# Kernel tuning notes

Hardware: AMD Instinct MI355X
Metric: run time of the kernel (lower is better)

The kernel has to match this reference:

```python
import jax, jax.numpy as jnp
import numpy as np

H = 8          # n_channels
NEIGHBORS = 5


def setup_inputs() -> dict:
    key = jax.random.key(0)
    k1, k2 = jax.random.split(key)
    B, N, C = 8, 1024, 256
    x = jax.random.normal(k1, (B, N, C), dtype=jnp.float32)
    # torch Linear weight: [out_features, in_features] = [2*H*C, C]
    W_qk = jax.random.normal(k2, (2 * H * C, C), dtype=jnp.float32) * (C ** -0.5)
    return {"x": x, "W_qk": W_qk}


def _forward(x, W_qk):
    B, N, C = x.shape
    scale = C ** -0.5
    qk = (x @ W_qk.T).reshape(B, N, 2, H, C).transpose(2, 0, 3, 1, 4)
    q, k = qk[0], qk[1]                              # [B,H,N,C]
    attn = jax.nn.softmax(jnp.einsum('bhnc,bhmc->bhnm', q, k) * scale, axis=-1)

    # clip(): top-k on detached channel-summed attention
    sum_edge = jnp.sum(jax.lax.stop_gradient(attn), axis=1)   # [B,N,N]
    _, index = jax.lax.top_k(sum_edge, NEIGHBORS)             # [B,N,NEIGHBORS]
    # Faithful to source: every mask row gets 1 at the union of ALL rows'
    # top-k indices (inner loop iterates over all rows of `inds`), plus eye(N).
    flat_idx = index.reshape(B, N * NEIGHBORS)                # [B, N*nb]
    col_mask = jnp.zeros((B, N), dtype=attn.dtype).at[
        jnp.arange(B)[:, None], flat_idx].set(1.0)            # [B,N]
    mask = jnp.maximum(jnp.eye(N, dtype=attn.dtype)[None], col_mask[:, None, :])  # [B,N,N]

    new_edge = mask[:, None] * attn                           # [B,H,N,N]

    # norm_edge(): row norm, then col norm, then row @ col^T
    norm_row = new_edge / (jnp.sum(new_edge, axis=-1, keepdims=True) + 1e-16)
    norm_col = norm_row / (jnp.sum(norm_row, axis=-2, keepdims=True) + 1e-16)
    return jnp.einsum('bhnm,bhkm->bhnk', norm_row, norm_col)  # [B,H,N,N]


def reference(x, W_qk):
    return _forward(x, W_qk)
```

## Files before the change

### kernel.cpp

```cpp
#include <hip/hip_runtime.h>
#include <hip/hip_bf16.h>
#include <cstdint>
#include <cstddef>

#define BB 8
#define HH 8
#define NN 1024
#define CC 256
#define OUTCH 4096

typedef __attribute__((ext_vector_type(8))) __bf16 bf16x8;
typedef __attribute__((ext_vector_type(4))) __bf16 bf16x4;
typedef __attribute__((ext_vector_type(4))) float f32x4;

__device__ inline void async16(const void* g, void* l)
{
  __builtin_amdgcn_global_load_lds(
      reinterpret_cast<const __attribute__((address_space(1))) unsigned int*>(
          reinterpret_cast<uintptr_t>(g)),
      reinterpret_cast<__attribute__((address_space(3))) unsigned int*>(
          reinterpret_cast<uintptr_t>(l)),
      16, 0, 0);
}

__device__ inline float waveMax(float v) {
#pragma unroll
  for (int o = 32; o > 0; o >>= 1) v = fmaxf(v, __shfl_xor(v, o, 64));
  return v;
}
__device__ inline float waveSum(float v) {
#pragma unroll
  for (int o = 32; o > 0; o >>= 1) v += __shfl_xor(v, o, 64);
  return v;
}

__global__ __launch_bounds__(256) void split_kernel(const float* __restrict__ in,
                                                    __bf16* __restrict__ hi,
                                                    __bf16* __restrict__ lo, int n4)
{
  const int i = blockIdx.x * 256 + threadIdx.x;
  if (i >= n4) return;
  const float4 v = ((const float4*)in)[i];
  bf16x4 h, l;
  h.x = (__bf16)v.x; l.x = (__bf16)(v.x - (float)h.x);
  h.y = (__bf16)v.y; l.y = (__bf16)(v.y - (float)h.y);
  h.z = (__bf16)v.z; l.z = (__bf16)(v.z - (float)h.z);
  h.w = (__bf16)v.w; l.w = (__bf16)(v.w - (float)h.w);
  ((bf16x4*)hi)[i] = h;
  ((bf16x4*)lo)[i] = l;
}

__global__ __launch_bounds__(256) void xw_mfma_kernel(
    const __bf16* __restrict__ Ah, const __bf16* __restrict__ Al,
    const __bf16* __restrict__ Bh, const __bf16* __restrict__ Bl,
    __bf16* __restrict__ Chi, __bf16* __restrict__ Clo)
{
  __shared__ __bf16 AsH[128 * 32], AsL[128 * 32], BsH[128 * 32], BsL[128 * 32];

  const int tid = threadIdx.x, lane = tid & 63, wid = tid >> 6;
  const int wr = wid >> 1, wc = wid & 1;
  const int bM = blockIdx.y * 128, bN = blockIdx.x * 128;

  const int srow = wid * 16 + (lane >> 2);
  const int scol = (lane & 3) * 8;
  const __bf16* gAh = Ah + (size_t)(bM + srow) * CC + scol;
  const __bf16* gAl = Al + (size_t)(bM + srow) * CC + scol;
  const __bf16* gBh = Bh + (size_t)(bN + srow) * CC + scol;
  const __bf16* gBl = Bl + (size_t)(bN + srow) * CC + scol;
  char* lAh = (char*)AsH + wid * 16 * 64;
  char* lAl = (char*)AsL + wid * 16 * 64;
  char* lBh = (char*)BsH + wid * 16 * 64;
  char* lBl = (char*)BsL + wid * 16 * 64;

  f32x4 acc[4][4];
  const f32x4 z = {0.f, 0.f, 0.f, 0.f};
#pragma unroll
  for (int m = 0; m < 4; ++m)
#pragma unroll
    for (int n = 0; n < 4; ++n) acc[m][n] = z;

  for (int k0 = 0; k0 < CC; k0 += 32) {
    async16(gAh + k0, lAh); async16(gAh + k0 + 64 * CC, lAh + 64 * 64);
    async16(gAl + k0, lAl); async16(gAl + k0 + 64 * CC, lAl + 64 * 64);
    async16(gBh + k0, lBh); async16(gBh + k0 + 64 * CC, lBh + 64 * 64);
    async16(gBl + k0, lBl); async16(gBl + k0 + 64 * CC, lBl + 64 * 64);
    __syncthreads();

    bf16x8 ah[4], al[4], bh_[4], bl_[4];
    const int fb = (lane & 15) * 64 + (lane >> 4) * 16;
#pragma unroll
    for (int m = 0; m < 4; ++m) {
      ah[m] = *(const bf16x8*)((const char*)AsH + (wr * 64 + m * 16) * 64 + fb);
      al[m] = *(const bf16x8*)((const char*)AsL + (wr * 64 + m * 16) * 64 + fb);
    }
#pragma unroll
    for (int n = 0; n < 4; ++n) {
      bh_[n] = *(const bf16x8*)((const char*)BsH + (wc * 64 + n * 16) * 64 + fb);
      bl_[n] = *(const bf16x8*)((const char*)BsL + (wc * 64 + n * 16) * 64 + fb);
    }
#pragma unroll
    for (int m = 0; m < 4; ++m)
#pragma unroll
      for (int n = 0; n < 4; ++n) {
        acc[m][n] = __builtin_amdgcn_mfma_f32_16x16x32_bf16(al[m], bh_[n], acc[m][n], 0, 0, 0);
        acc[m][n] = __builtin_amdgcn_mfma_f32_16x16x32_bf16(ah[m], bl_[n], acc[m][n], 0, 0, 0);
        acc[m][n] = __builtin_amdgcn_mfma_f32_16x16x32_bf16(ah[m], bh_[n], acc[m][n], 0, 0, 0);
      }
    __syncthreads();
  }

  const int fr = lane & 15;
  const int fq = lane >> 4;
#pragma unroll
  for (int m = 0; m < 4; ++m) {
    const int row0 = bM + wr * 64 + m * 16 + fq * 4;
#pragma unroll
    for (int n = 0; n < 4; ++n) {
      const int col = bN + wc * 64 + n * 16 + fr;
#pragma unroll
      for (int r = 0; r < 4; ++r) {
        const float v = acc[m][n][r];
        const __bf16 h = (__bf16)v;
        const __bf16 l = (__bf16)(v - (float)h);
        Chi[(size_t)(row0 + r) * OUTCH + col] = h;
        Clo[(size_t)(row0 + r) * OUTCH + col] = l;
      }
    }
  }
}

__global__ __launch_bounds__(256) void qkt_mfma_kernel(
    const __bf16* __restrict__ Qh, const __bf16* __restrict__ Ql,
    float* __restrict__ outall)
{
  const int f = blockIdx.x;
  const int xcd = f & 7;
  const int g = f >> 3;
  const int bh = xcd + 8 * (g >> 6);
  const int tile = g & 63;
  const int b = bh >> 3, h = bh & 7;
  const size_t qoff = (size_t)b * NN * OUTCH + (size_t)h * CC;
  const size_t koff = qoff + 2048;
  float* C = outall + ((size_t)bh << 20);

  __shared__ __bf16 AsH[128 * 32], AsL[128 * 32], BsH[128 * 32], BsL[128 * 32];

  const int tid = threadIdx.x, lane = tid & 63, wid = tid >> 6;
  const int wr = wid >> 1, wc = wid & 1;
  const int bM = (tile >> 3) * 128, bN = (tile & 7) * 128;

  const int srow = wid * 16 + (lane >> 2);
  const int scol = (lane & 3) * 8;
  const __bf16* gAh = Qh + qoff + (size_t)(bM + srow) * OUTCH + scol;
  const __bf16* gAl = Ql + qoff + (size_t)(bM + srow) * OUTCH + scol;
  const __bf16* gBh = Qh + koff + (size_t)(bN + srow) * OUTCH + scol;
  const __bf16* gBl = Ql + koff + (size_t)(bN + srow) * OUTCH + scol;
  char* lAh = (char*)AsH + wid * 16 * 64;
  char* lAl = (char*)AsL + wid * 16 * 64;
  char* lBh = (char*)BsH + wid * 16 * 64;
  char* lBl = (char*)BsL + wid * 16 * 64;

  f32x4 acc[4][4];
  const f32x4 z = {0.f, 0.f, 0.f, 0.f};
#pragma unroll
  for (int m = 0; m < 4; ++m)
#pragma unroll
    for (int n = 0; n < 4; ++n) acc[m][n] = z;

  for (int k0 = 0; k0 < CC; k0 += 32) {
    async16(gAh + k0, lAh); async16(gAh + k0 + (size_t)64 * OUTCH, lAh + 64 * 64);
    async16(gAl + k0, lAl); async16(gAl + k0 + (size_t)64 * OUTCH, lAl + 64 * 64);
    async16(gBh + k0, lBh); async16(gBh + k0 + (size_t)64 * OUTCH, lBh + 64 * 64);
    async16(gBl + k0, lBl); async16(gBl + k0 + (size_t)64 * OUTCH, lBl + 64 * 64);
    __syncthreads();

    bf16x8 ah[4], al[4], bh_[4], bl_[4];
    const int fb = (lane & 15) * 64 + (lane >> 4) * 16;
#pragma unroll
    for (int m = 0; m < 4; ++m) {
      ah[m] = *(const bf16x8*)((const char*)AsH + (wr * 64 + m * 16) * 64 + fb);
      al[m] = *(const bf16x8*)((const char*)AsL + (wr * 64 + m * 16) * 64 + fb);
    }
#pragma unroll
    for (int n = 0; n < 4; ++n) {
      bh_[n] = *(const bf16x8*)((const char*)BsH + (wc * 64 + n * 16) * 64 + fb);
      bl_[n] = *(const bf16x8*)((const char*)BsL + (wc * 64 + n * 16) * 64 + fb);
    }
#pragma unroll
    for (int m = 0; m < 4; ++m)
#pragma unroll
      for (int n = 0; n < 4; ++n) {
        acc[m][n] = __builtin_amdgcn_mfma_f32_16x16x32_bf16(al[m], bh_[n], acc[m][n], 0, 0, 0);
        acc[m][n] = __builtin_amdgcn_mfma_f32_16x16x32_bf16(ah[m], bl_[n], acc[m][n], 0, 0, 0);
        acc[m][n] = __builtin_amdgcn_mfma_f32_16x16x32_bf16(ah[m], bh_[n], acc[m][n], 0, 0, 0);
      }
    __syncthreads();
  }

  const int fr = lane & 15;
  const int fq = lane >> 4;
#pragma unroll
  for (int m = 0; m < 4; ++m) {
    const int row0 = bM + wr * 64 + m * 16 + fq * 4;
#pragma unroll
    for (int n = 0; n < 4; ++n) {
      const int col = bN + wc * 64 + n * 16 + fr;
#pragma unroll
      for (int r = 0; r < 4; ++r)
        C[(size_t)(row0 + r) * NN + col] = acc[m][n][r] * 0.0625f;
    }
  }
}

__global__ __launch_bounds__(256) void softmax_se_kernel(float* __restrict__ attn,
                                                         float* __restrict__ se)
{
  const int bn = blockIdx.x;
  const int b = bn >> 10;
  const int n = bn & 1023;
  const int t = threadIdx.x;
  const int lane = t & 63, wv = t >> 6;
  __shared__ float wred[4];
  float* base = attn + ((size_t)b * HH * NN + n) * NN;
  __bf16* baseb = (__bf16*)base;
  float4 acc = make_float4(0.f, 0.f, 0.f, 0.f);

#pragma unroll 1
  for (int h = 0; h < HH; ++h) {
    float* ar = base + (size_t)h * NN * NN;
    __bf16* arb = baseb + (size_t)h * NN * NN * 2;
    float4 x = *(float4*)(ar + (t << 2));
    float mx = waveMax(fmaxf(fmaxf(x.x, x.y), fmaxf(x.z, x.w)));
    if (lane == 0) wred[wv] = mx;
    __syncthreads();
    const float M = fmaxf(fmaxf(wred[0], wred[1]), fmaxf(wred[2], wred[3]));
    __syncthreads();

    float e0 = expf(x.x - M), e1 = expf(x.y - M), e2 = expf(x.z - M), e3 = expf(x.w - M);
    float s = waveSum(e0 + e1 + e2 + e3);
    if (lane == 0) wred[wv] = s;
    __syncthreads();
    const float inv = 1.0f / (wred[0] + wred[1] + wred[2] + wred[3]);

    const float o0 = e0 * inv, o1 = e1 * inv, o2 = e2 * inv, o3 = e3 * inv;
    bf16x4 ob; ob.x = (__bf16)o0; ob.y = (__bf16)o1; ob.z = (__bf16)o2; ob.w = (__bf16)o3;
    *(bf16x4*)(arb + (t << 2)) = ob;
    acc.x += o0; acc.y += o1; acc.z += o2; acc.w += o3;
    __syncthreads();
  }
  *(float4*)(se + (size_t)bn * NN + (t << 2)) = acc;
}

__global__ __launch_bounds__(256) void topk_kernel(const float* __restrict__ se,
                                                   float* __restrict__ colmask)
{
  const int bn = blockIdx.x;
  const int b = bn >> 10;
  const int t = threadIdx.x;
  __shared__ float vals[NN];
  __shared__ unsigned long long red[256];
  const float* rowp = se + (size_t)bn * NN;
  for (int i = t; i < NN; i += 256) vals[i] = rowp[i];
  __syncthreads();

  for (int it = 0; it < 5; ++it) {
    unsigned long long best = 0ull;
    for (int i = t; i < NN; i += 256) {
      const float v = vals[i];
      if (v >= 0.f) {
        unsigned long long key =
            ((unsigned long long)__float_as_uint(v) << 32) | (unsigned)(NN - 1 - i);
        if (key > best) best = key;
      }
    }
    red[t] = best; __syncthreads();
    for (int s = 128; s > 0; s >>= 1) {
      if (t < s) red[t] = red[t] > red[t+s] ? red[t] : red[t+s];
      __syncthreads();
    }
    if (t == 0) {
      const int idx = NN - 1 - (int)(red[0] & 0xFFFFFFFFull);
      colmask[b * NN + idx] = 1.0f;
      vals[idx] = -1.0f;
    }
    __syncthreads();
  }
}

__global__ __launch_bounds__(256) void rs_kernel(const __bf16* __restrict__ attnb,
                                                 const float* __restrict__ colmask,
                                                 float* __restrict__ inv_rs)
{
  const int row = blockIdx.x;
  const int n = row & 1023;
  const int bh = row >> 10;
  const int b = bh >> 3;
  const int t = threadIdx.x;
  const int lane = t & 63, wv = t >> 6;
  const __bf16* ar = attnb + (size_t)row * 2048;
  const float* cm = colmask + b * NN;
  const int m = t << 2;
  const bf16x4 vb = *(const bf16x4*)(ar + m);
  const float4 c = *(const float4*)(cm + m);
  float acc = 0.f;
  acc += ((c.x != 0.f) || (m + 0 == n)) ? (float)vb.x : 0.f;
  acc += ((c.y != 0.f) || (m + 1 == n)) ? (float)vb.y : 0.f;
  acc += ((c.z != 0.f) || (m + 2 == n)) ? (float)vb.z : 0.f;
  acc += ((c.w != 0.f) || (m + 3 == n)) ? (float)vb.w : 0.f;
  acc = waveSum(acc);
  __shared__ float wred[4];
  if (lane == 0) wred[wv] = acc;
  __syncthreads();
  if (t == 0) inv_rs[row] = 1.0f / (wred[0] + wred[1] + wred[2] + wred[3] + 1e-16f);
}

__global__ __launch_bounds__(256) void cs_part_kernel(const __bf16* __restrict__ attnb,
                                                      const float* __restrict__ colmask,
                                                      const float* __restrict__ inv_rs,
                                                      float* __restrict__ part)
{
  const int bh = blockIdx.y;
  const int b = bh >> 3;
  const int chunk = blockIdx.x;
  const int m0 = threadIdx.x << 2;
  const __bf16* ab = attnb + (size_t)bh * NN * 2048;
  const float* ir = inv_rs + bh * NN;
  const float4 cm = *(const float4*)(colmask + b * NN + m0);
  float a0 = 0.f, a1 = 0.f, a2 = 0.f, a3 = 0.f;
  const int n0 = chunk * 128, n1 = n0 + 128;
  for (int n = n0; n < n1; ++n) {
    const bf16x4 vb = *(const bf16x4*)(ab + (size_t)n * 2048 + m0);
    const float w = ir[n];
    a0 += ((cm.x != 0.f) || (m0 + 0 == n)) ? (float)vb.x * w : 0.f;
    a1 += ((cm.y != 0.f) || (m0 + 1 == n)) ? (float)vb.y * w : 0.f;
    a2 += ((cm.z != 0.f) || (m0 + 2 == n)) ? (float)vb.z * w : 0.f;
    a3 += ((cm.w != 0.f) || (m0 + 3 == n)) ? (float)vb.w * w : 0.f;
  }
  float4 o; o.x = a0; o.y = a1; o.z = a2; o.w = a3;
  *(float4*)(part + ((size_t)chunk * BB * HH + bh) * NN + m0) = o;
}

__global__ __launch_bounds__(256) void cs_fin_kernel(const float* __restrict__ part,
                                                     float* __restrict__ isc)
{
  const int bh = blockIdx.x;
  const int m0 = threadIdx.x << 2;
  float a0 = 0.f, a1 = 0.f, a2 = 0.f, a3 = 0.f;
#pragma unroll
  for (int c = 0; c < 8; ++c) {
    const float4 p = *(const float4*)(part + ((size_t)c * BB * HH + bh) * NN + m0);
    a0 += p.x; a1 += p.y; a2 += p.z; a3 += p.w;
  }
  float4 o;
  o.x = 1.0f / sqrtf(a0 + 1e-16f);
  o.y = 1.0f / sqrtf(a1 + 1e-16f);
  o.z = 1.0f / sqrtf(a2 + 1e-16f);
  o.w = 1.0f / sqrtf(a3 + 1e-16f);
  *(float4*)(isc + (size_t)bh * NN + m0) = o;
}

__global__ __launch_bounds__(256) void g_kernel(const __bf16* __restrict__ attnb,
                                                const float* __restrict__ colmask,
                                                const float* __restrict__ inv_rs,
                                                const float* __restrict__ isc,
                                                __bf16* __restrict__ Gb)
{
  const size_t idx = ((size_t)blockIdx.x * 256 + threadIdx.x) << 2;
  const size_t row = idx >> 10;
  const int m = (int)(idx & 1023);
  const int n = (int)(row & 1023);
  const int bh = (int)(row >> 10);
  const int b = bh >> 3;
  const bf16x4 vb = *(const bf16x4*)(attnb + row * 2048 + m);
  const float4 c = *(const float4*)(colmask + b * NN + m);
  const float4 s = *(const float4*)(isc + bh * NN + m);
  const float ir = inv_rs[row];
  bf16x4 o;
  o.x = (__bf16)((((c.x != 0.f) || (m + 0 == n)) ? (float)vb.x : 0.f) * ir * s.x);
  o.y = (__bf16)((((c.y != 0.f) || (m + 1 == n)) ? (float)vb.y : 0.f) * ir * s.y);
  o.z = (__bf16)((((c.z != 0.f) || (m + 2 == n)) ? (float)vb.z : 0.f) * ir * s.z);
  o.w = (__bf16)((((c.w != 0.f) || (m + 3 == n)) ? (float)vb.w : 0.f) * ir * s.w);
  *(bf16x4*)(Gb + idx) = o;
}

__global__ __launch_bounds__(256) void ggt_mfma_kernel(const __bf16* __restrict__ Gball,
                                                       float* __restrict__ outall)
{
  const int f = blockIdx.x;
  const int xcd = f & 7;
  const int g = f >> 3;
  const int bh = xcd + 8 * (g / 36);
  int tt = g % 36;

  const __bf16* A = Gball + ((size_t)bh << 20);
  float* C = outall + ((size_t)bh << 20);

  int ti = 0;
#pragma unroll
  for (int r = 0; r < 8; ++r) {
    const int len = 8 - r;
    if (tt < len) { ti = r; break; }
    tt -= len;
  }
  const int tj = ti + tt;

  __shared__ __bf16 As[128 * 32];
  __shared__ __bf16 Bs[128 * 32];

  const int tid  = threadIdx.x;
  const int lane = tid & 63;
  const int wid  = tid >> 6;
  const int wr   = wid >> 1;
  const int wc   = wid & 1;
  const int bM   = ti * 128;
  const int bN   = tj * 128;

  const int srow = wid * 16 + (lane >> 2);
  const int scol = (lane & 3) * 8;
  const __bf16* gA = A + (size_t)(bM + srow) * NN + scol;
  const __bf16* gB = A + (size_t)(bN + srow) * NN + scol;
  char* lA = (char*)As + wid * 16 * 64;
  char* lB = (char*)Bs + wid * 16 * 64;

  f32x4 acc[4][4];
  const f32x4 z = {0.f, 0.f, 0.f, 0.f};
#pragma unroll
  for (int m = 0; m < 4; ++m)
#pragma unroll
    for (int n = 0; n < 4; ++n) acc[m][n] = z;

  for (int k0 = 0; k0 < NN; k0 += 32) {
    async16(gA + k0,           lA);
    async16(gA + k0 + 64 * NN, lA + 64 * 64);
    async16(gB + k0,           lB);
    async16(gB + k0 + 64 * NN, lB + 64 * 64);
    __syncthreads();

    bf16x8 a[4], b[4];
    const int fb = (lane & 15) * 64 + (lane >> 4) * 16;
#pragma unroll
    for (int m = 0; m < 4; ++m)
      a[m] = *(const bf16x8*)((const char*)As + (wr * 64 + m * 16) * 64 + fb);
#pragma unroll
    for (int n = 0; n < 4; ++n)
      b[n] = *(const bf16x8*)((const char*)Bs + (wc * 64 + n * 16) * 64 + fb);
#pragma unroll
    for (int m = 0; m < 4; ++m)
#pragma unroll
      for (int n = 0; n < 4; ++n)
        acc[m][n] = __builtin_amdgcn_mfma_f32_16x16x32_bf16(a[m], b[n], acc[m][n], 0, 0, 0);
    __syncthreads();
  }

  const int fr = lane & 15;
  const int fq = lane >> 4;
#pragma unroll
  for (int m = 0; m < 4; ++m) {
    const int row0 = bM + wr * 64 + m * 16 + fq * 4;
#pragma unroll
    for (int n = 0; n < 4; ++n) {
      const int col = bN + wc * 64 + n * 16 + fr;
#pragma unroll
      for (int r = 0; r < 4; ++r)
        C[(size_t)(row0 + r) * NN + col] = acc[m][n][r];
    }
  }
  if (ti != tj) {
#pragma unroll
    for (int m = 0; m < 4; ++m) {
      const int colT = bM + wr * 64 + m * 16 + fq * 4;
#pragma unroll
      for (int n = 0; n < 4; ++n) {
        const int rowT = bN + wc * 64 + n * 16 + fr;
        *(f32x4*)(C + (size_t)rowT * NN + colT) = acc[m][n];
      }
    }
  }
}

extern "C" void kernel_launch(void* const* d_in, const int* in_sizes, int n_in,
                              void* d_out, int out_size, void* d_ws, size_t ws_size,
                              hipStream_t stream)
{
  const float* x = (const float*)d_in[0];
  const float* W = (const float*)d_in[1];
  float* attn = (float*)d_out;
  __bf16* attnb = (__bf16*)d_out;
  char* ws = (char*)d_ws;

  __bf16* qk_hi = (__bf16*)(ws + ((size_t)0   << 20));
  __bf16* qk_lo = (__bf16*)(ws + ((size_t)64  << 20));
  __bf16* Gb    = (__bf16*)(ws + ((size_t)0   << 20));
  __bf16* x_hi  = (__bf16*)(ws + ((size_t)128 << 20));
  __bf16* x_lo  = (__bf16*)(ws + ((size_t)132 << 20));
  __bf16* W_hi  = (__bf16*)(ws + ((size_t)136 << 20));
  __bf16* W_lo  = (__bf16*)(ws + ((size_t)138 << 20));
  float*  se    = (float*)(ws + ((size_t)144 << 20));
  float*  cmask = (float*)(ws + ((size_t)176 << 20));
  float*  irs   = (float*)(ws + ((size_t)177 << 20));
  float*  isc   = (float*)(ws + ((size_t)178 << 20));
  float*  csp   = (float*)(ws + ((size_t)180 << 20));

  hipLaunchKernelGGL(split_kernel, dim3((BB*NN*CC/4 + 255)/256), dim3(256), 0, stream,
                     x, x_hi, x_lo, BB*NN*CC/4);
  hipLaunchKernelGGL(split_kernel, dim3((OUTCH*CC/4 + 255)/256), dim3(256), 0, stream,
                     W, W_hi, W_lo, OUTCH*CC/4);

  hipLaunchKernelGGL(xw_mfma_kernel, dim3(OUTCH/128, (BB*NN)/128, 1), dim3(256), 0, stream,
                     x_hi, x_lo, W_hi, W_lo, qk_hi, qk_lo);

  hipLaunchKernelGGL(qkt_mfma_kernel, dim3(64 * 64), dim3(256), 0, stream,
                     qk_hi, qk_lo, attn);

  hipLaunchKernelGGL(softmax_se_kernel, dim3(BB*NN), dim3(256), 0, stream, attn, se);

  hipMemsetAsync(cmask, 0, (size_t)BB * NN * 4, stream);
  hipLaunchKernelGGL(topk_kernel, dim3(BB*NN), dim3(256), 0, stream, se, cmask);

  hipLaunchKernelGGL(rs_kernel, dim3(BB*HH*NN), dim3(256), 0, stream, attnb, cmask, irs);

  hipLaunchKernelGGL(cs_part_kernel, dim3(8, BB*HH), dim3(256), 0, stream,
                     attnb, cmask, irs, csp);
  hipLaunchKernelGGL(cs_fin_kernel, dim3(BB*HH), dim3(256), 0, stream, csp, isc);

  hipLaunchKernelGGL(g_kernel, dim3((BB*HH*NN*(long long)NN) / 4 / 256), dim3(256), 0, stream,
                     attnb, cmask, irs, isc, Gb);

  hipLaunchKernelGGL(ggt_mfma_kernel, dim3(36 * 64), dim3(256), 0, stream,
                     Gb, attn);

  (void)in_sizes; (void)n_in; (void)out_size; (void)ws_size;
}
```

Before: 586.3 us.

## Fuse row/column normalization and fold masked scaling into GGT operand load

Softmax now writes dense bf16 probabilities to a workspace buffer instead of in place into strided output rows. The row-sum pass is merged into the column-partial kernel, and the separate G materialization kernel is removed. The GGT matmul now loads attention directly and applies the mask, row scale and column scale while staging tiles into LDS. This removes a full read and write of the B*H*N*N matrix and two launches. The cost is synchronous register loads in place of async global-to-LDS copies, plus extra ALU work in the matmul inner loop.

After: 577.4 us. About the same (-1.5%).

```diff
diff --git a/kernel.cpp b/kernel.cpp
--- a/kernel.cpp
+++ b/kernel.cpp
@@ -212,7 +212,8 @@
   }
 }
 
-__global__ __launch_bounds__(256) void softmax_se_kernel(float* __restrict__ attn,
+__global__ __launch_bounds__(256) void softmax_se_kernel(const float* __restrict__ logits,
+                                                         __bf16* __restrict__ attnb,
                                                          float* __restrict__ se)
 {
   const int bn = blockIdx.x;
@@ -221,15 +222,14 @@
   const int t = threadIdx.x;
   const int lane = t & 63, wv = t >> 6;
   __shared__ float wred[4];
-  float* base = attn + ((size_t)b * HH * NN + n) * NN;
-  __bf16* baseb = (__bf16*)base;
   float4 acc = make_float4(0.f, 0.f, 0.f, 0.f);
 
 #pragma unroll 1
   for (int h = 0; h < HH; ++h) {
-    float* ar = base + (size_t)h * NN * NN;
-    __bf16* arb = baseb + (size_t)h * NN * NN * 2;
-    float4 x = *(float4*)(ar + (t << 2));
+    const size_t rowbase = (((size_t)(b * HH + h) << 10) + n) << 10;
+    const float* ar = logits + rowbase;
+    __bf16* arb = attnb + rowbase;
+    float4 x = *(const float4*)(ar + (t << 2));
     float mx = waveMax(fmaxf(fmaxf(x.x, x.y), fmaxf(x.z, x.w)));
     if (lane == 0) wred[wv] = mx;
     __syncthreads();
@@ -287,68 +287,81 @@
   }
 }
 
-__global__ __launch_bounds__(256) void rs_kernel(const __bf16* __restrict__ attnb,
-                                                 const float* __restrict__ colmask,
-                                                 float* __restrict__ inv_rs)
-{
-  const int row = blockIdx.x;
-  const int n = row & 1023;
-  const int bh = row >> 10;
-  const int b = bh >> 3;
-  const int t = threadIdx.x;
-  const int lane = t & 63, wv = t >> 6;
-  const __bf16* ar = attnb + (size_t)row * 2048;
-  const float* cm = colmask + b * NN;
-  const int m = t << 2;
-  const bf16x4 vb = *(const bf16x4*)(ar + m);
-  const float4 c = *(const float4*)(cm + m);
-  float acc = 0.f;
-  acc += ((c.x != 0.f) || (m + 0 == n)) ? (float)vb.x : 0.f;
-  acc += ((c.y != 0.f) || (m + 1 == n)) ? (float)vb.y : 0.f;
-  acc += ((c.z != 0.f) || (m + 2 == n)) ? (float)vb.z : 0.f;
-  acc += ((c.w != 0.f) || (m + 3 == n)) ? (float)vb.w : 0.f;
-  acc = waveSum(acc);
-  __shared__ float wred[4];
-  if (lane == 0) wred[wv] = acc;
-  __syncthreads();
-  if (t == 0) inv_rs[row] = 1.0f / (wred[0] + wred[1] + wred[2] + wred[3] + 1e-16f);
-}
-
-__global__ __launch_bounds__(256) void cs_part_kernel(const __bf16* __restrict__ attnb,
-                                                      const float* __restrict__ colmask,
-                                                      const float* __restrict__ inv_rs,
-                                                      float* __restrict__ part)
+__global__ __launch_bounds__(256) void cs_rs_kernel(const __bf16* __restrict__ attnb,
+                                                    const float* __restrict__ colmask,
+                                                    float* __restrict__ inv_rs,
+                                                    float* __restrict__ part)
 {
   const int bh = blockIdx.y;
   const int b = bh >> 3;
   const int chunk = blockIdx.x;
-  const int m0 = threadIdx.x << 2;
-  const __bf16* ab = attnb + (size_t)bh * NN * 2048;
-  const float* ir = inv_rs + bh * NN;
-  const float4 cm = *(const float4*)(colmask + b * NN + m0);
-  float a0 = 0.f, a1 = 0.f, a2 = 0.f, a3 = 0.f;
-  const int n0 = chunk * 128, n1 = n0 + 128;
-  for (int n = n0; n < n1; ++n) {
-    const bf16x4 vb = *(const bf16x4*)(ab + (size_t)n * 2048 + m0);
-    const float w = ir[n];
-    a0 += ((cm.x != 0.f) || (m0 + 0 == n)) ? (float)vb.x * w : 0.f;
-    a1 += ((cm.y != 0.f) || (m0 + 1 == n)) ? (float)vb.y * w : 0.f;
-    a2 += ((cm.z != 0.f) || (m0 + 2 == n)) ? (float)vb.z * w : 0.f;
-    a3 += ((cm.w != 0.f) || (m0 + 3 == n)) ? (float)vb.w * w : 0.f;
-  }
-  float4 o; o.x = a0; o.y = a1; o.z = a2; o.w = a3;
-  *(float4*)(part + ((size_t)chunk * BB * HH + bh) * NN + m0) = o;
+  const int t = threadIdx.x, lane = t & 63, wv = t >> 6;
+  const __bf16* ab = attnb + ((size_t)bh << 20);
+  const float* cm = colmask + b * NN;
+  const int c0 = lane * 16;
+
+  float cmv[16];
+#pragma unroll
+  for (int q = 0; q < 4; ++q) {
+    const float4 c4 = *(const float4*)(cm + c0 + q * 4);
+    cmv[q*4+0] = c4.x; cmv[q*4+1] = c4.y; cmv[q*4+2] = c4.z; cmv[q*4+3] = c4.w;
+  }
+
+  float a[16];
+#pragma unroll
+  for (int j = 0; j < 16; ++j) a[j] = 0.f;
+
+  const int nbase = chunk * 64 + wv * 16;
+#pragma unroll 1
+  for (int r = 0; r < 16; ++r) {
+    const int n = nbase + r;
+    const __bf16* rowp = ab + ((size_t)n << 10) + c0;
+    const bf16x8 v0 = *(const bf16x8*)(rowp);
+    const bf16x8 v1 = *(const bf16x8*)(rowp + 8);
+    float e[16];
+    float rsum = 0.f;
+#pragma unroll
+    for (int j = 0; j < 8; ++j) {
+      const float val = ((cmv[j] != 0.f) || (c0 + j == n)) ? (float)v0[j] : 0.f;
+      e[j] = val; rsum += val;
+    }
+#pragma unroll
+    for (int j = 0; j < 8; ++j) {
+      const float val = ((cmv[8+j] != 0.f) || (c0 + 8 + j == n)) ? (float)v1[j] : 0.f;
+      e[8+j] = val; rsum += val;
+    }
+    rsum = waveSum(rsum);
+    const float ir = 1.0f / (rsum + 1e-16f);
+    if (lane == 0) inv_rs[bh * NN + n] = ir;
+#pragma unroll
+    for (int j = 0; j < 16; ++j) a[j] += e[j] * ir;
+  }
+
+  __shared__ float l[4][NN];
+#pragma unroll
+  for (int j = 0; j < 16; ++j) l[wv][c0 + j] = a[j];
+  __syncthreads();
+  const int m0 = t << 2;
+  float4 o;
+  o.x = l[0][m0+0] + l[1][m0+0] + l[2][m0+0] + l[3][m0+0];
+  o.y = l[0][m0+1] + l[1][m0+1] + l[2][m0+1] + l[3][m0+1];
+  o.z = l[0][m0+2] + l[1][m0+2] + l[2][m0+2] + l[3][m0+2];
+  o.w = l[0][m0+3] + l[1][m0+3] + l[2][m0+3] + l[3][m0+3];
+  *(float4*)(part + (((size_t)chunk * (BB*HH) + bh) << 10) + m0) = o;
 }
 
 __global__ __launch_bounds__(256) void cs_fin_kernel(const float* __restrict__ part,
-                                                     float* __restrict__ isc)
+                                                     const float* __restrict__ colmask,
+                                                     float* __restrict__ isc,
+                                                     float* __restrict__ sel0)
 {
   const int bh = blockIdx.x;
+  const int b = bh >> 3;
   const int m0 = threadIdx.x << 2;
   float a0 = 0.f, a1 = 0.f, a2 = 0.f, a3 = 0.f;
 #pragma unroll
-  for (int c = 0; c < 8; ++c) {
-    const float4 p = *(const float4*)(part + ((size_t)c * BB * HH + bh) * NN + m0);
+  for (int c = 0; c < 16; ++c) {
+    const float4 p = *(const float4*)(part + (((size_t)c * (BB*HH) + bh) << 10) + m0);
     a0 += p.x; a1 += p.y; a2 += p.z; a3 += p.w;
   }
   float4 o;
@@ -356,34 +369,20 @@
   o.y = 1.0f / sqrtf(a1 + 1e-16f);
   o.z = 1.0f / sqrtf(a2 + 1e-16f);
   o.w = 1.0f / sqrtf(a3 + 1e-16f);
-  *(float4*)(isc + (size_t)bh * NN + m0) = o;
-}
-
-__global__ __launch_bounds__(256) void g_kernel(const __bf16* __restrict__ attnb,
-                                                const float* __restrict__ colmask,
-                                                const float* __restrict__ inv_rs,
-                                                const float* __restrict__ isc,
-                                                __bf16* __restrict__ Gb)
-{
-  const size_t idx = ((size_t)blockIdx.x * 256 + threadIdx.x) << 2;
-  const size_t row = idx >> 10;
-  const int m = (int)(idx & 1023);
-  const int n = (int)(row & 1023);
-  const int bh = (int)(row >> 10);
-  const int b = bh >> 3;
-  const bf16x4 vb = *(const bf16x4*)(attnb + row * 2048 + m);
-  const float4 c = *(const float4*)(colmask + b * NN + m);
-  const float4 s = *(const float4*)(isc + bh * NN + m);
-  const float ir = inv_rs[row];
-  bf16x4 o;
-  o.x = (__bf16)((((c.x != 0.f) || (m + 0 == n)) ? (float)vb.x : 0.f) * ir * s.x);
-  o.y = (__bf16)((((c.y != 0.f) || (m + 1 == n)) ? (float)vb.y : 0.f) * ir * s.y);
-  o.z = (__bf16)((((c.z != 0.f) || (m + 2 == n)) ? (float)vb.z : 0.f) * ir * s.z);
-  o.w = (__bf16)((((c.w != 0.f) || (m + 3 == n)) ? (float)vb.w : 0.f) * ir * s.w);
-  *(bf16x4*)(Gb + idx) = o;
-}
-
-__global__ __launch_bounds__(256) void ggt_mfma_kernel(const __bf16* __restrict__ Gball,
+  *(float4*)(isc + ((size_t)bh << 10) + m0) = o;
+  const float4 cm = *(const float4*)(colmask + b * NN + m0);
+  float4 s;
+  s.x = (cm.x != 0.f) ? o.x : 0.f;
+  s.y = (cm.y != 0.f) ? o.y : 0.f;
+  s.z = (cm.z != 0.f) ? o.z : 0.f;
+  s.w = (cm.w != 0.f) ? o.w : 0.f;
+  *(float4*)(sel0 + ((size_t)bh << 10) + m0) = s;
+}
+
+__global__ __launch_bounds__(256) void ggt_mfma_kernel(const __bf16* __restrict__ attnb,
+                                                       const float* __restrict__ irs,
+                                                       const float* __restrict__ iscb,
+                                                       const float* __restrict__ sel0b,
                                                        float* __restrict__ outall)
 {
   const int f = blockIdx.x;
@@ -392,7 +391,10 @@
   const int bh = xcd + 8 * (g / 36);
   int tt = g % 36;
 
-  const __bf16* A = Gball + ((size_t)bh << 20);
+  const __bf16* A = attnb + ((size_t)bh << 20);
+  const float* ir = irs + bh * NN;
+  const float* isc = iscb + ((size_t)bh << 10);
+  const float* sel0 = sel0b + ((size_t)bh << 10);
   float* C = outall + ((size_t)bh << 20);
 
   int ti = 0;
@@ -417,10 +419,10 @@
 
   const int srow = wid * 16 + (lane >> 2);
   const int scol = (lane & 3) * 8;
-  const __bf16* gA = A + (size_t)(bM + srow) * NN + scol;
-  const __bf16* gB = A + (size_t)(bN + srow) * NN + scol;
-  char* lA = (char*)As + wid * 16 * 64;
-  char* lB = (char*)Bs + wid * 16 * 64;
+
+  const int rA0 = bM + srow, rA1 = bM + 64 + srow;
+  const int rB0 = bN + srow, rB1 = bN + 64 + srow;
+  const float irA0 = ir[rA0], irA1 = ir[rA1], irB0 = ir[rB0], irB1 = ir[rB1];
 
   f32x4 acc[4][4];
   const f32x4 z = {0.f, 0.f, 0.f, 0.f};
@@ -430,10 +432,32 @@
     for (int n = 0; n < 4; ++n) acc[m][n] = z;
 
   for (int k0 = 0; k0 < NN; k0 += 32) {
-    async16(gA + k0,           lA);
-    async16(gA + k0 + 64 * NN, lA + 64 * 64);
-    async16(gB + k0,           lB);
-    async16(gB + k0 + 64 * NN, lB + 64 * 64);
+    const int kc = k0 + scol;
+    const float4 i0 = *(const float4*)(isc + kc);
+    const float4 i1 = *(const float4*)(isc + kc + 4);
+    const float4 s0 = *(const float4*)(sel0 + kc);
+    const float4 s1 = *(const float4*)(sel0 + kc + 4);
+    const float iv[8] = {i0.x, i0.y, i0.z, i0.w, i1.x, i1.y, i1.z, i1.w};
+    const float sv[8] = {s0.x, s0.y, s0.z, s0.w, s1.x, s1.y, s1.z, s1.w};
+
+    const bf16x8 vA0 = *(const bf16x8*)(A + ((size_t)rA0 << 10) + kc);
+    const bf16x8 vA1 = *(const bf16x8*)(A + ((size_t)rA1 << 10) + kc);
+    const bf16x8 vB0 = *(const bf16x8*)(A + ((size_t)rB0 << 10) + kc);
+    const bf16x8 vB1 = *(const bf16x8*)(A + ((size_t)rB1 << 10) + kc);
+
+    bf16x8 gA0, gA1, gB0, gB1;
+#pragma unroll
+    for (int j = 0; j < 8; ++j) {
+      const int k = kc + j;
+      gA0[j] = (__bf16)((float)vA0[j] * irA0 * ((k == rA0) ? iv[j] : sv[j]));
+      gA1[j] = (__bf16)((float)vA1[j] * irA1 * ((k == rA1) ? iv[j] : sv[j]));
+      gB0[j] = (__bf16)((float)vB0[j] * irB0 * ((k == rB0) ? iv[j] : sv[j]));
+      gB1[j] = (__bf16)((float)vB1[j] * irB1 * ((k == rB1) ? iv[j] : sv[j]));
+    }
+    *(bf16x8*)(&As[srow * 32 + scol])        = gA0;
+    *(bf16x8*)(&As[(64 + srow) * 32 + scol]) = gA1;
+    *(bf16x8*)(&Bs[srow * 32 + scol])        = gB0;
+    *(bf16x8*)(&Bs[(64 + srow) * 32 + scol]) = gB1;
     __syncthreads();
 
     bf16x8 a[4], b[4];
@@ -484,13 +508,12 @@
 {
   const float* x = (const float*)d_in[0];
   const float* W = (const float*)d_in[1];
-  float* attn = (float*)d_out;
-  __bf16* attnb = (__bf16*)d_out;
+  float* logits = (float*)d_out;
   char* ws = (char*)d_ws;
 
   __bf16* qk_hi = (__bf16*)(ws + ((size_t)0   << 20));
   __bf16* qk_lo = (__bf16*)(ws + ((size_t)64  << 20));
-  __bf16* Gb    = (__bf16*)(ws + ((size_t)0   << 20));
+  __bf16* attnb = (__bf16*)(ws + ((size_t)0   << 20));
   __bf16* x_hi  = (__bf16*)(ws + ((size_t)128 << 20));
   __bf16* x_lo  = (__bf16*)(ws + ((size_t)132 << 20));
   __bf16* W_hi  = (__bf16*)(ws + ((size_t)136 << 20));
@@ -499,6 +522,7 @@
   float*  cmask = (float*)(ws + ((size_t)176 << 20));
   float*  irs   = (float*)(ws + ((size_t)177 << 20));
   float*  isc   = (float*)(ws + ((size_t)178 << 20));
+  float*  sel0  = (float*)(ws + ((size_t)179 << 20));
   float*  csp   = (float*)(ws + ((size_t)180 << 20));
 
   hipLaunchKernelGGL(split_kernel, dim3((BB*NN*CC/4 + 255)/256), dim3(256), 0, stream,
@@ -510,24 +534,21 @@
                      x_hi, x_lo, W_hi, W_lo, qk_hi, qk_lo);
 
   hipLaunchKernelGGL(qkt_mfma_kernel, dim3(64 * 64), dim3(256), 0, stream,
-                     qk_hi, qk_lo, attn);
-
-  hipLaunchKernelGGL(softmax_se_kernel, dim3(BB*NN), dim3(256), 0, stream, attn, se);
+                     qk_hi, qk_lo, logits);
+
+  hipLaunchKernelGGL(softmax_se_kernel, dim3(BB*NN), dim3(256), 0, stream,
+                     logits, attnb, se);
 
   hipMemsetAsync(cmask, 0, (size_t)BB * NN * 4, stream);
   hipLaunchKernelGGL(topk_kernel, dim3(BB*NN), dim3(256), 0, stream, se, cmask);
 
-  hipLaunchKernelGGL(rs_kernel, dim3(BB*HH*NN), dim3(256), 0, stream, attnb, cmask, irs);
-
-  hipLaunchKernelGGL(cs_part_kernel, dim3(8, BB*HH), dim3(256), 0, stream,
+  hipLaunchKernelGGL(cs_rs_kernel, dim3(16, BB*HH), dim3(256), 0, stream,
                      attnb, cmask, irs, csp);
-  hipLaunchKernelGGL(cs_fin_kernel, dim3(BB*HH), dim3(256), 0, stream, csp, isc);
-
-  hipLaunchKernelGGL(g_kernel, dim3((BB*HH*NN*(long long)NN) / 4 / 256), dim3(256), 0, stream,
-                     attnb, cmask, irs, isc, Gb);
+  hipLaunchKernelGGL(cs_fin_kernel, dim3(BB*HH), dim3(256), 0, stream,
+                     csp, cmask, isc, sel0);
 
   hipLaunchKernelGGL(ggt_mfma_kernel, dim3(36 * 64), dim3(256), 0, stream,
-                     Gb, attn);
+                     attnb, irs, isc, sel0, logits);
 
   (void)in_sizes; (void)n_in; (void)out_size; (void)ws_size;
 }
```
